# Kernel tuning notes

Hardware: AMD Instinct MI355X
Metric: run time of the kernel (lower is better)

The kernel has to match this reference:

```python
import jax, jax.numpy as jnp
import numpy as np

D_MODEL = 1024
N_HEADS = 16
D_HEAD = D_MODEL // N_HEADS


def setup_inputs() -> dict:
    key = jax.random.key(0)
    ks = jax.random.split(key, 9)
    s = 1.0 / np.sqrt(D_MODEL)
    def lin(kw, kb):
        W = jax.random.uniform(kw, (D_MODEL, D_MODEL), jnp.float32, -s, s)
        b = jax.random.uniform(kb, (D_MODEL,), jnp.float32, -s, s)
        return W, b
    Wq, bq = lin(ks[0], ks[1])
    Wk, bk = lin(ks[2], ks[3])
    Wv, bv = lin(ks[4], ks[5])
    Wo, bo = lin(ks[6], ks[7])
    x = jax.random.normal(ks[8], (4, 2048, D_MODEL), jnp.float32)
    return {"x": x, "Wq": Wq, "bq": bq, "Wk": Wk, "bk": bk,
            "Wv": Wv, "bv": bv, "Wo": Wo, "bo": bo}


def reference(x, Wq, bq, Wk, bk, Wv, bv, Wo, bo):
    B, T, C = x.shape
    # torch Linear: y = x @ W.T + b
    Q = x @ Wq.T + bq
    K = x @ Wk.T + bk
    V = x @ Wv.T + bv
    # [B, H, T, Dh]
    Q = Q.reshape(B, T, N_HEADS, D_HEAD).transpose(0, 2, 1, 3)
    K = K.reshape(B, T, N_HEADS, D_HEAD).transpose(0, 2, 1, 3)
    V = V.reshape(B, T, N_HEADS, D_HEAD).transpose(0, 2, 1, 3)
    scale = jnp.float32(np.sqrt(D_HEAD))
    scores = jnp.einsum('bhqd,bhkd->bhqk', Q, K) / scale
    causal = jnp.tril(jnp.ones((T, T), dtype=bool))  # True where allowed
    scores = jnp.where(causal, scores, jnp.float32(-jnp.inf))
    attn = jax.nn.softmax(scores, axis=-1)
    out = jnp.einsum('bhqk,bhkd->bhqd', attn, V)
    out = out.transpose(0, 2, 1, 3).reshape(B, T, C)
    return out @ Wo.T + bo
```

## Files before the change

kernel.cpp:

```cpp
#include <hip/hip_runtime.h>
#include <hip/hip_bf16.h>


typedef float f32x4 __attribute__((ext_vector_type(4)));
typedef __bf16 bf16x8 __attribute__((ext_vector_type(8)));

#define DEVI __device__ __forceinline__

#define QSCALE 0.1803368801111204f

template<int N> struct IC { static constexpr int value = N; };

DEVI ushort f2b(float x) {
  __hip_bfloat16 h = __float2bfloat16(x);
  return __builtin_bit_cast(ushort, h);
}

DEVI unsigned int pkbf(float a, float b) {
#if __has_builtin(__builtin_amdgcn_cvt_pk_bf16_f32)
  typedef __bf16 bf16x2 __attribute__((ext_vector_type(2)));
  bf16x2 r = __builtin_amdgcn_cvt_pk_bf16_f32(a, b);
  return __builtin_bit_cast(unsigned int, r);
#else
  return (unsigned int)f2b(a) | ((unsigned int)f2b(b) << 16);
#endif
}

DEVI bf16x8 ldsFrag(const ushort* p) {
  return __builtin_bit_cast(bf16x8, *(const uint4*)p);
}

DEVI f32x4 mfma16(bf16x8 a, bf16x8 b, f32x4 c) {
  return __builtin_amdgcn_mfma_f32_16x16x32_bf16(a, b, c, 0, 0, 0);
}

DEVI void gload_lds16(const ushort* g, ushort* l) {
  __builtin_amdgcn_global_load_lds(
      (const __attribute__((address_space(1))) unsigned int*)g,
      (__attribute__((address_space(3))) unsigned int*)l, 16, 0, 0);
}

__global__ void k_cvtAll(const float4* __restrict__ x,
                         const float4* __restrict__ w0, const float4* __restrict__ w1,
                         const float4* __restrict__ w2, const float4* __restrict__ w3,
                         ushort4* __restrict__ xb, ushort4* __restrict__ wcat) {
  const int blk = blockIdx.x;
  const int i = blk * 256 + threadIdx.x;
  float4 f;
  ushort4* dst;
  int di;
  if (blk < 8192) {
    f = x[i]; dst = xb; di = i;
  } else {
    const int wi = i - 8192 * 256;
    const int sel = wi >> 18;
    const float4* src = (sel == 0) ? w0 : (sel == 1) ? w1 : (sel == 2) ? w2 : w3;
    f = src[wi & 262143]; dst = wcat; di = wi;
  }
  ushort4 o;
  o.x = f2b(f.x); o.y = f2b(f.y); o.z = f2b(f.z); o.w = f2b(f.w);
  dst[di] = o;
}

template<int MODE>
__global__ __launch_bounds__(256)
void k_gemm(const ushort* __restrict__ A, const ushort* __restrict__ W,
            const float* __restrict__ b0, const float* __restrict__ b1,
            const float* __restrict__ b2, float* __restrict__ outF,
            ushort* __restrict__ oQ, ushort* __restrict__ oK, ushort* __restrict__ oV) {
  __shared__ ushort As[128 * 64];
  __shared__ ushort Bs[128 * 64];
  const int tid = threadIdx.x;
  const int wave = tid >> 6, lane = tid & 63;
  const int col = lane & 15, quad = lane >> 4;
  const int id = blockIdx.x;
  const int s_ = id >> 3;
  const int m0 = ((id & 7) * 8 + (s_ & 7)) * 128;
  const int n0 = (s_ >> 3) * 128;
  const int wm = (wave >> 1) * 64, wn = (wave & 1) * 64;
  f32x4 acc[4][4] = {};

  const int grow = lane >> 3;
  const int gchunk = ((lane & 7) ^ grow) * 8;
  const ushort* Ag = A + (size_t)(m0 + wave * 8 + grow) * 1024 + gchunk;
  const ushort* Wg = W + (size_t)(n0 + wave * 8 + grow) * 1024 + gchunk;
  ushort* AsW = &As[wave * 512];
  ushort* BsW = &Bs[wave * 512];

  const int matId = (MODE == 0) ? (n0 >> 10) : 0;
  const int cswz = col & 7;

  auto kloop = [&](auto swc) {
    constexpr bool SW = (decltype(swc)::value != 0);
    for (int k0 = 0; k0 < 1024; k0 += 64) {
      __syncthreads();
#pragma unroll
      for (int g = 0; g < 4; ++g) {
        gload_lds16(Ag + (size_t)g * 32 * 1024 + k0, AsW + g * 2048);
        gload_lds16(Wg + (size_t)g * 32 * 1024 + k0, BsW + g * 2048);
      }
      __syncthreads();
#pragma unroll
      for (int kk = 0; kk < 2; ++kk) {
        bf16x8 af[4], bfr[4];
#pragma unroll
        for (int i = 0; i < 4; ++i)
          af[i] = ldsFrag(&As[(wm + i * 16 + col) * 64 + (((kk * 4 + quad) ^ cswz) * 8)]);
#pragma unroll
        for (int j = 0; j < 4; ++j)
          bfr[j] = ldsFrag(&Bs[(wn + j * 16 + col) * 64 + (((kk * 4 + quad) ^ cswz) * 8)]);
#pragma unroll
        for (int i = 0; i < 4; ++i)
#pragma unroll
          for (int j = 0; j < 4; ++j) {
            if constexpr (SW)
              acc[i][j] = mfma16(bfr[j], af[i], acc[i][j]);
            else
              acc[i][j] = mfma16(af[i], bfr[j], acc[i][j]);
          }
      }
    }
  };

  if (MODE == 1 || matId < 2) kloop(IC<1>{}); else kloop(IC<0>{});

  if (MODE == 1) {
#pragma unroll
    for (int j = 0; j < 4; ++j) {
      const int nb = n0 + wn + j * 16 + quad * 4;
      const float4 bb = *(const float4*)&b0[nb];
#pragma unroll
      for (int i = 0; i < 4; ++i) {
        const int m = m0 + wm + i * 16 + col;
        float4 v;
        v.x = acc[i][j][0] + bb.x;
        v.y = acc[i][j][1] + bb.y;
        v.z = acc[i][j][2] + bb.z;
        v.w = acc[i][j][3] + bb.w;
        *(float4*)&outF[(size_t)m * 1024 + nb] = v;
      }
    }
  } else if (matId < 2) {
    ushort* dst = (matId == 0) ? oQ : oK;
    const float* bias = (matId == 0) ? b0 : b1;
    const float sc = (matId == 0) ? QSCALE : 1.0f;
#pragma unroll
    for (int j = 0; j < 4; ++j) {
      const int nl = ((n0 & 1023) + wn + j * 16 + quad * 4);
      const int h = nl >> 6, dh0 = nl & 63;
      const float4 bb = *(const float4*)&bias[nl];
#pragma unroll
      for (int i = 0; i < 4; ++i) {
        const int m = m0 + wm + i * 16 + col;
        const int b = m >> 11, t = m & 2047;
        ushort4 pk;
        pk.x = f2b((acc[i][j][0] + bb.x) * sc);
        pk.y = f2b((acc[i][j][1] + bb.y) * sc);
        pk.z = f2b((acc[i][j][2] + bb.z) * sc);
        pk.w = f2b((acc[i][j][3] + bb.w) * sc);
        *(ushort4*)&dst[(((size_t)(b * 16 + h) * 2048) + t) * 64 + dh0] = pk;
      }
    }
  } else {
#pragma unroll
    for (int j = 0; j < 4; ++j) {
      const int nl = ((n0 & 1023) + wn + j * 16 + col);
      const int h = nl >> 6, dh = nl & 63;
      const float bn = b2[nl];
#pragma unroll
      for (int i = 0; i < 4; ++i) {
        const int mBase = m0 + wm + i * 16 + quad * 4;
        const int b = mBase >> 11, t = mBase & 2047;
        ushort4 pk;
        pk.x = f2b(acc[i][j][0] + bn);
        pk.y = f2b(acc[i][j][1] + bn);
        pk.z = f2b(acc[i][j][2] + bn);
        pk.w = f2b(acc[i][j][3] + bn);
        *(ushort4*)&oV[(((size_t)(b * 16 + h) * 64) + dh) * 2048 + t] = pk;
      }
    }
  }
}

__global__ __launch_bounds__(512, 1)
void k_attn(const ushort* __restrict__ Q, const ushort* __restrict__ K,
            const ushort* __restrict__ Vt, ushort* __restrict__ AO) {
  __shared__ ushort Ks[2 * 4096];
  __shared__ ushort Vs[2 * 4096];
  __shared__ ushort Os[512];
  __shared__ ushort Ps[16 * 16 * 72];
  const int tid = threadIdx.x;
  const int wave = tid >> 6, lane = tid & 63;
  const int col = lane & 15, quad = lane >> 4;
  const int id = blockIdx.x;
  const int bh = (id & 7) * 8 + ((id >> 3) & 7);
  const int pr = id >> 6;
  const ushort* Qg = Q + (size_t)bh * 2048 * 64;
  const ushort* Kg = K + (size_t)bh * 2048 * 64;
  const ushort* Vg = Vt + (size_t)bh * 64 * 2048;

  if (tid < 128) {
    const ushort one = 0x3F80;
    ushort4 zv;
    if (tid < 8) { zv.x = one; zv.y = one; zv.z = one; zv.w = one; }
    else         { zv.x = 0;   zv.y = 0;   zv.z = 0;   zv.w = 0;   }
    *(ushort4*)&Os[tid * 4] = zv;
  }

  const int grow = lane >> 3;
  const int gchunk = ((lane & 7) ^ grow) * 8;
  const int cswz = col & 7;
  ushort* Pw0 = &Ps[((wave * 2 + 0) * 16 + col) * 72];
  ushort* Pw1 = &Ps[((wave * 2 + 1) * 16 + col) * 72];

  for (int pp = 0; pp < 2; ++pp) {
    const int t = pp ? (7 - pr) : pr;
    const int q0 = t * 256;

    bf16x8 qf[2][2];
#pragma unroll
    for (int s = 0; s < 2; ++s) {
      const ushort* p = Qg + (q0 + wave * 32 + s * 16 + col) * 64 + quad * 8;
      qf[s][0] = __builtin_bit_cast(bf16x8, *(const uint4*)p);
      qf[s][1] = __builtin_bit_cast(bf16x8, *(const uint4*)(p + 32));
    }

    f32x4 o[2][4] = {};
    f32x4 la[2] = {};

    const ushort* kPtr = Kg + (wave * 8 + grow) * 64 + gchunk;
    const ushort* vPtr = Vg + (size_t)(wave * 8 + grow) * 2048 + gchunk;

    auto stage = [&](auto bufc) {
      constexpr int BUF = decltype(bufc)::value;
      gload_lds16(kPtr, &Ks[BUF * 4096 + wave * 512]);
      gload_lds16(vPtr, &Vs[BUF * 4096 + wave * 512]);
      kPtr += 64 * 64;
      vPtr += 64;
    };

    auto step = [&](auto bufc, auto maskc, int j0) {
      constexpr int BUF = decltype(bufc)::value;
      constexpr bool MASKED = (decltype(maskc)::value != 0);
      const ushort* Kb = &Ks[BUF * 4096];
      const ushort* Vb = &Vs[BUF * 4096];
      bf16x8 kf[4][2];
#pragma unroll
      for (int i = 0; i < 4; ++i) {
        kf[i][0] = ldsFrag(&Kb[(i * 16 + col) * 64 + (((0 * 4 + quad) ^ cswz) * 8)]);
        kf[i][1] = ldsFrag(&Kb[(i * 16 + col) * 64 + (((1 * 4 + quad) ^ cswz) * 8)]);
      }
#pragma unroll
      for (int s = 0; s < 2; ++s) {
        ushort* Pw = s ? Pw1 : Pw0;
        const int dlim = MASKED ? (q0 + wave * 32 + s * 16 + col - j0 - quad * 4) : 0;
#pragma unroll
        for (int i = 0; i < 4; ++i) {
          f32x4 z = {0.f, 0.f, 0.f, 0.f};
          f32x4 sv = mfma16(kf[i][0], qf[s][0], z);
          sv = mfma16(kf[i][1], qf[s][1], sv);
          if (MASKED) {
#pragma unroll
            for (int r = 0; r < 4; ++r)
              if (i * 16 + r > dlim) sv[r] = -1e30f;
          }
          f32x4 pv;
#pragma unroll
          for (int r = 0; r < 4; ++r) pv[r] = __builtin_amdgcn_exp2f(sv[r]);
          uint2 pk;
          pk.x = pkbf(pv[0], pv[1]);
          pk.y = pkbf(pv[2], pv[3]);
          *(uint2*)&Pw[i * 16 + quad * 4] = pk;
        }
      }
      bf16x8 osf = ldsFrag(&Os[col * 32 + quad * 8]);
#pragma unroll
      for (int c = 0; c < 2; ++c) {
        bf16x8 pb0 = ldsFrag(&Pw0[c * 32 + quad * 8]);
        bf16x8 pb1 = ldsFrag(&Pw1[c * 32 + quad * 8]);
        la[0] = mfma16(osf, pb0, la[0]);
        la[1] = mfma16(osf, pb1, la[1]);
#pragma unroll
        for (int i = 0; i < 4; ++i) {
          bf16x8 vf = ldsFrag(&Vb[(i * 16 + col) * 64 + (((c * 4 + quad) ^ cswz) * 8)]);
          o[0][i] = mfma16(vf, pb0, o[0][i]);
          o[1][i] = mfma16(vf, pb1, o[1][i]);
        }
      }
    };

    __syncthreads();
    stage(IC<0>{});
    for (int it2 = 0; it2 < 2 * t; ++it2) {
      __syncthreads();
      stage(IC<1>{});
      step(IC<0>{}, IC<0>{}, 0);
      __syncthreads();
      stage(IC<0>{});
      step(IC<1>{}, IC<0>{}, 0);
    }
    __syncthreads();
    stage(IC<1>{});
    step(IC<0>{}, IC<1>{}, q0);
    __syncthreads();
    stage(IC<0>{});
    if (wave >= 2) step(IC<1>{}, IC<1>{}, q0 + 64);
    __syncthreads();
    stage(IC<1>{});
    if (wave >= 4) step(IC<0>{}, IC<1>{}, q0 + 128);
    __syncthreads();
    if (wave >= 6) step(IC<1>{}, IC<1>{}, q0 + 192);

    const float invs[2] = {1.0f / __shfl(la[0][0], col), 1.0f / __shfl(la[1][0], col)};
    const int b = bh >> 4, h = bh & 15;
#pragma unroll
    for (int s = 0; s < 2; ++s) {
      const float inv = invs[s];
      const int tq = q0 + wave * 32 + s * 16 + col;
      ushort* dst = AO + (size_t)(b * 2048 + tq) * 1024 + h * 64;
#pragma unroll
      for (int i = 0; i < 4; ++i) {
        f32x4 v = o[s][i];
        ushort4 pk;
        pk.x = f2b(v[0] * inv);
        pk.y = f2b(v[1] * inv);
        pk.z = f2b(v[2] * inv);
        pk.w = f2b(v[3] * inv);
        *(ushort4*)&dst[i * 16 + quad * 4] = pk;
      }
    }
  }
}

extern "C" void kernel_launch(void* const* d_in, const int* in_sizes, int n_in,
                              void* d_out, int out_size, void* d_ws, size_t ws_size,
                              hipStream_t stream) {
  const float* x  = (const float*)d_in[0];
  const float* Wq = (const float*)d_in[1];
  const float* bq = (const float*)d_in[2];
  const float* Wk = (const float*)d_in[3];
  const float* bk = (const float*)d_in[4];
  const float* Wv = (const float*)d_in[5];
  const float* bv = (const float*)d_in[6];
  const float* Wo = (const float*)d_in[7];
  const float* bo = (const float*)d_in[8];
  float* out = (float*)d_out;

  char* ws = (char*)d_ws;
  ushort* xb    = (ushort*)ws;
  ushort* Wcat  = (ushort*)(ws + (size_t)16 * 1024 * 1024);
  ushort* Wob   = Wcat + (size_t)3 * 1024 * 1024;
  ushort* Qh    = (ushort*)(ws + (size_t)24 * 1024 * 1024);
  ushort* Kh    = Qh + (size_t)8192 * 1024;
  ushort* Vt    = Kh + (size_t)8192 * 1024;
  ushort* AO    = Vt + (size_t)8192 * 1024;

  k_cvtAll<<<12288, 256, 0, stream>>>((const float4*)x,
                                      (const float4*)Wq, (const float4*)Wk,
                                      (const float4*)Wv, (const float4*)Wo,
                                      (ushort4*)xb, (ushort4*)Wcat);

  k_gemm<0><<<1536, 256, 0, stream>>>(xb, Wcat, bq, bk, bv, nullptr, Qh, Kh, Vt);

  k_attn<<<256, 512, 0, stream>>>(Qh, Kh, Vt, AO);

  k_gemm<1><<<512, 256, 0, stream>>>(AO, Wob, bo, nullptr, nullptr, out,
                                     nullptr, nullptr, nullptr);
}
```

Measured before the change: 249.0 us.

## Prefetch next GEMM K-tile into registers while computing current tile

Replaces the direct global-to-LDS loads with register-staged loads: the next K-tile's global reads are issued before the MFMA loop, and the values are written into shared memory after a barrier. This is meant to hide global memory latency behind compute with a single LDS buffer. In exchange it adds extra VGPR pressure and explicit LDS store instructions in place of the async LDS-load path.

Result: no change. 252.0 us (+1.2%).

```diff
diff --git a/kernel.cpp b/kernel.cpp
--- a/kernel.cpp
+++ b/kernel.cpp
@@ -62,6 +62,26 @@
   dst[di] = o;
 }
 
+#define GLOAD(k0)                                          \
+  pa0 = *(const uint4*)(Ag + (k0));                        \
+  pa1 = *(const uint4*)(Ag + 32 * 1024 + (k0));            \
+  pa2 = *(const uint4*)(Ag + 64 * 1024 + (k0));            \
+  pa3 = *(const uint4*)(Ag + 96 * 1024 + (k0));            \
+  pb0 = *(const uint4*)(Wg + (k0));                        \
+  pb1 = *(const uint4*)(Wg + 32 * 1024 + (k0));            \
+  pb2 = *(const uint4*)(Wg + 64 * 1024 + (k0));            \
+  pb3 = *(const uint4*)(Wg + 96 * 1024 + (k0));
+
+#define SWRITE()                                           \
+  *(uint4*)(AsW)        = pa0;                             \
+  *(uint4*)(AsW + 2048) = pa1;                             \
+  *(uint4*)(AsW + 4096) = pa2;                             \
+  *(uint4*)(AsW + 6144) = pa3;                             \
+  *(uint4*)(BsW)        = pb0;                             \
+  *(uint4*)(BsW + 2048) = pb1;                             \
+  *(uint4*)(BsW + 4096) = pb2;                             \
+  *(uint4*)(BsW + 6144) = pb3;
+
 template<int MODE>
 __global__ __launch_bounds__(256)
 void k_gemm(const ushort* __restrict__ A, const ushort* __restrict__ W,
@@ -84,22 +104,20 @@
   const int gchunk = ((lane & 7) ^ grow) * 8;
   const ushort* Ag = A + (size_t)(m0 + wave * 8 + grow) * 1024 + gchunk;
   const ushort* Wg = W + (size_t)(n0 + wave * 8 + grow) * 1024 + gchunk;
-  ushort* AsW = &As[wave * 512];
-  ushort* BsW = &Bs[wave * 512];
+  ushort* AsW = &As[wave * 512 + lane * 8];
+  ushort* BsW = &Bs[wave * 512 + lane * 8];
 
   const int matId = (MODE == 0) ? (n0 >> 10) : 0;
   const int cswz = col & 7;
 
   auto kloop = [&](auto swc) {
     constexpr bool SW = (decltype(swc)::value != 0);
-    for (int k0 = 0; k0 < 1024; k0 += 64) {
+    uint4 pa0, pa1, pa2, pa3, pb0, pb1, pb2, pb3;
+    GLOAD(0);
+    SWRITE();
+    for (int it = 0; it < 16; ++it) {
       __syncthreads();
-#pragma unroll
-      for (int g = 0; g < 4; ++g) {
-        gload_lds16(Ag + (size_t)g * 32 * 1024 + k0, AsW + g * 2048);
-        gload_lds16(Wg + (size_t)g * 32 * 1024 + k0, BsW + g * 2048);
-      }
-      __syncthreads();
+      if (it + 1 < 16) { GLOAD((it + 1) * 64); }
 #pragma unroll
       for (int kk = 0; kk < 2; ++kk) {
         bf16x8 af[4], bfr[4];
@@ -119,6 +137,8 @@
               acc[i][j] = mfma16(af[i], bfr[j], acc[i][j]);
           }
       }
+      __syncthreads();
+      if (it + 1 < 16) { SWRITE(); }
     }
   };
 
```
